# Kernel tuning notes

Measured on AMD Instinct MI355X. Metric: run time of the kernel, lower is better.

Reference implementation:

```python
import jax, jax.numpy as jnp
import numpy as np

B, N, C = 2, 2048, 1024
H = 16
D = C // H  # head_dim = 64
SCALE = D ** -0.5


def setup_inputs() -> dict:
    key = jax.random.key(0)
    k1, k2, k3, k4 = jax.random.split(key, 4)
    x = jax.random.normal(k1, (B, N, C), dtype=jnp.float32)
    # nn.Linear(in_dim, 3*out_dim, bias=False): store as [in, 3*out] for x @ W
    w_qkv = jax.random.normal(k2, (C, 3 * C), dtype=jnp.float32) * (C ** -0.5)
    w_proj = jax.random.normal(k3, (C, C), dtype=jnp.float32) * (C ** -0.5)
    b_proj = jax.random.normal(k4, (C,), dtype=jnp.float32) * 0.01
    return {"x": x, "w_qkv": w_qkv, "w_proj": w_proj, "b_proj": b_proj}


def reference(x, w_qkv, w_proj, b_proj):
    b, n, c = x.shape
    # QKV projection -> [3, B, H, N, D]
    qkv = (x @ w_qkv).reshape(b, n, 3, H, D).transpose(2, 0, 3, 1, 4)
    q, k, v = qkv[0], qkv[1], qkv[2]
    # scaled dot-product attention, full [B, H, N, N] scores as in original
    attn = jax.nn.softmax(jnp.einsum('bhqd,bhkd->bhqk', q * SCALE, k), axis=-1)
    out = jnp.einsum('bhqk,bhkd->bhqd', attn, v)  # [B, H, N, D]
    out = out.transpose(0, 2, 1, 3).reshape(b, n, c)
    return out @ w_proj + b_proj
```

## Files before the change

kernel.cpp:

```cpp
#include <hip/hip_runtime.h>

typedef unsigned short u16;
typedef float f32x4 __attribute__((ext_vector_type(4)));
typedef short bf16x8 __attribute__((ext_vector_type(8)));
typedef u16 u16x4 __attribute__((ext_vector_type(4)));
typedef u16 u16x8 __attribute__((ext_vector_type(8)));
typedef __bf16 bfr4 __attribute__((ext_vector_type(4)));

#define BB 2
#define NN 2048
#define CC 1024
#define HH 16
#define DD 64
#define MM (BB * NN)
#define NQKV (3 * CC)
#define QSCALE 0.18033688011112042f

#if __has_builtin(__builtin_amdgcn_exp2f)
#define EXP2(x) __builtin_amdgcn_exp2f(x)
#else
#define EXP2(x) exp2f(x)
#endif

__device__ __forceinline__ u16 f2bf(float f) {
    unsigned u = __float_as_uint(f);
    u += 0x7FFFu + ((u >> 16) & 1u);
    return (u16)(u >> 16);
}

__device__ __forceinline__ void ld_lds16(const u16* g, u16* l) {
    __builtin_amdgcn_global_load_lds(
        (const __attribute__((address_space(1))) unsigned int*)g,
        (__attribute__((address_space(3))) unsigned int*)l, 16, 0, 0);
}

__global__ __launch_bounds__(256) void k_tobf(const float* __restrict__ in,
                                              u16* __restrict__ out, int n) {
    int i = (blockIdx.x * 256 + threadIdx.x) * 8;
    if (i >= n) return;
    float4 a = *(const float4*)(in + i);
    float4 b = *(const float4*)(in + i + 4);
    u16x8 o;
    o[0] = f2bf(a.x); o[1] = f2bf(a.y); o[2] = f2bf(a.z); o[3] = f2bf(a.w);
    o[4] = f2bf(b.x); o[5] = f2bf(b.y); o[6] = f2bf(b.z); o[7] = f2bf(b.w);
    *(u16x8*)(out + i) = o;
}

__global__ __launch_bounds__(256) void k_tcast(const float* __restrict__ in,
                                               u16* __restrict__ out,
                                               int K, int Nn) {
    __shared__ float tile[32][33];
    int t = threadIdx.x, tx = t & 31, ty = t >> 5;
    int n0 = blockIdx.x * 32, k0 = blockIdx.y * 32;
#pragma unroll
    for (int r = 0; r < 32; r += 8)
        tile[ty + r][tx] = in[(size_t)(k0 + ty + r) * Nn + n0 + tx];
    __syncthreads();
#pragma unroll
    for (int r = 0; r < 32; r += 8)
        out[(size_t)(n0 + ty + r) * K + k0 + tx] = f2bf(tile[tx][ty + r]);
}

template <int MODE>
__global__ __launch_bounds__(256) void k_gemm(
    const u16* __restrict__ A, const u16* __restrict__ B,
    u16* __restrict__ Qb, u16* __restrict__ Kb, u16* __restrict__ Vb,
    const float* __restrict__ bias, float* __restrict__ Cout) {
    const int Kd = 1024;
    __shared__ __align__(16) u16 Ah[128][32];
    __shared__ __align__(16) u16 Bh[128][32];

    int t = threadIdx.x;
    int wave = t >> 6, lane = t & 63;
    int quad = lane >> 4, l16 = lane & 15;
    int wm = (wave >> 1) * 64, wn = (wave & 1) * 64;
    int m0 = blockIdx.y * 128, n0 = blockIdx.x * 128;

    int strow0 = wave * 16 + (lane >> 2);
    int stdst  = (lane & 3) * 8;
    int stsrc  = ((lane & 3) ^ ((lane >> 3) & 3)) * 8;
    int cfrag = (quad ^ ((l16 >> 1) & 3)) * 8;

    f32x4 acc[4][4];
#pragma unroll
    for (int i = 0; i < 4; i++)
#pragma unroll
        for (int j = 0; j < 4; j++) acc[i][j] = f32x4{0.f, 0.f, 0.f, 0.f};

    for (int k0 = 0; k0 < Kd; k0 += 32) {
        __syncthreads();
#pragma unroll
        for (int ii = 0; ii < 2; ii++) {
            int row = strow0 + ii * 64;
            ld_lds16(A + (size_t)(m0 + row) * Kd + k0 + stsrc, &Ah[row][stdst]);
            ld_lds16(B + (size_t)(n0 + row) * Kd + k0 + stsrc, &Bh[row][stdst]);
        }
        __syncthreads();

        bf16x8 af[4], bf[4];
#pragma unroll
        for (int i = 0; i < 4; i++) {
            af[i] = *(const bf16x8*)&Ah[wm + i * 16 + l16][cfrag];
            bf[i] = *(const bf16x8*)&Bh[wn + i * 16 + l16][cfrag];
        }
#pragma unroll
        for (int mi = 0; mi < 4; mi++)
#pragma unroll
            for (int ni = 0; ni < 4; ni++)
                acc[mi][ni] = __builtin_amdgcn_mfma_f32_16x16x32_bf16(
                    af[mi], bf[ni], acc[mi][ni], 0, 0, 0);
    }

#pragma unroll
    for (int mi = 0; mi < 4; mi++)
#pragma unroll
        for (int ni = 0; ni < 4; ni++)
#pragma unroll
            for (int r = 0; r < 4; r++) {
                int grow = m0 + wm + mi * 16 + quad * 4 + r;
                int gcol = n0 + wn + ni * 16 + l16;
                float v = acc[mi][ni][r];
                if (MODE == 0) {
                    int three = gcol >> 10, rem = gcol & 1023;
                    int h = rem >> 6, d = rem & 63;
                    int bb = grow >> 11, nn = grow & 2047;
                    if (three == 0) {
                        Qb[((size_t)(bb * HH + h) * NN + nn) * DD + d] = f2bf(v * QSCALE);
                    } else if (three == 1) {
                        Kb[((size_t)(bb * HH + h) * NN + nn) * DD + d] = f2bf(v);
                    } else {
                        Vb[((size_t)(bb * HH + h) * DD + d) * NN + nn] = f2bf(v);
                    }
                } else {
                    Cout[(size_t)grow * CC + gcol] = v + bias[gcol];
                }
            }
}

__global__ __launch_bounds__(512) void k_attn(const u16* __restrict__ Qb,
                                              const u16* __restrict__ Kb,
                                              const u16* __restrict__ VbT,
                                              u16* __restrict__ Ob) {
    __shared__ __align__(16) u16 Ks0[64][64], Ks1[64][64];
    __shared__ __align__(16) u16 Vs0[64][64], Vs1[64][64];
    __shared__ __align__(16) u16 Ps[8][16][72];

    int t = threadIdx.x, wave = t >> 6, lane = t & 63;
    int quad = lane >> 4, l16 = lane & 15;
    int bh = blockIdx.y, q0 = blockIdx.x * 128;
    const size_t kbase = (size_t)bh * NN * DD;
    const size_t vbase = (size_t)bh * DD * NN;

    int qrow = q0 + wave * 16 + l16;
    bf16x8 qf0 = *(const bf16x8*)&Qb[kbase + (size_t)qrow * DD + quad * 8];
    bf16x8 qf1 = *(const bf16x8*)&Qb[kbase + (size_t)qrow * DD + 32 + quad * 8];

    f32x4 o[4];
#pragma unroll
    for (int i = 0; i < 4; i++) o[i] = f32x4{0.f, 0.f, 0.f, 0.f};
    f32x4 lrow = f32x4{0.f, 0.f, 0.f, 0.f};

    int stgrp = lane & 7;
    int stsrc = (stgrp ^ (lane >> 3)) * 8;
    int strow = wave * 8 + (lane >> 3);
    int cf0 = (quad ^ (l16 & 7)) * 8;
    int cf1 = ((4 + quad) ^ (l16 & 7)) * 8;

    auto STAGE = [&](int cc, u16 (*Kd_)[64], u16 (*Vd_)[64]) {
        ld_lds16(&Kb[kbase + (size_t)(cc * 64 + strow) * DD + stsrc],
                 &Kd_[strow][stgrp * 8]);
        ld_lds16(&VbT[vbase + (size_t)strow * NN + cc * 64 + stsrc],
                 &Vd_[strow][stgrp * 8]);
    };

    auto COMPUTE = [&](u16 (*Ksrc)[64], u16 (*Vsrc)[64]) {
        bf16x8 kf[4][2];
#pragma unroll
        for (int kt = 0; kt < 4; kt++) {
            kf[kt][0] = *(const bf16x8*)&Ksrc[kt * 16 + l16][cf0];
            kf[kt][1] = *(const bf16x8*)&Ksrc[kt * 16 + l16][cf1];
        }
        f32x4 s[4];
        __builtin_amdgcn_s_setprio(1);
#pragma unroll
        for (int kt = 0; kt < 4; kt++) {
            f32x4 z = f32x4{0.f, 0.f, 0.f, 0.f};
            z = __builtin_amdgcn_mfma_f32_16x16x32_bf16(kf[kt][0], qf0, z, 0, 0, 0);
            z = __builtin_amdgcn_mfma_f32_16x16x32_bf16(kf[kt][1], qf1, z, 0, 0, 0);
            s[kt] = z;
        }
        __builtin_amdgcn_s_setprio(0);
#pragma unroll
        for (int kt = 0; kt < 4; kt++) {
            bfr4 pk;
#pragma unroll
            for (int r = 0; r < 4; r++) {
                float e = EXP2(s[kt][r]);
                lrow[r] += e;
                pk[r] = (__bf16)e;
            }
            *(bfr4*)&Ps[wave][l16][kt * 16 + quad * 4] = pk;
        }
        __asm__ volatile("s_waitcnt lgkmcnt(0)" ::: "memory");
        bf16x8 pb0 = *(const bf16x8*)&Ps[wave][l16][quad * 8];
        bf16x8 pb1 = *(const bf16x8*)&Ps[wave][l16][32 + quad * 8];
        __builtin_amdgcn_s_setprio(1);
#pragma unroll
        for (int dt = 0; dt < 4; dt++) {
            bf16x8 vf0 = *(const bf16x8*)&Vsrc[dt * 16 + l16][cf0];
            bf16x8 vf1 = *(const bf16x8*)&Vsrc[dt * 16 + l16][cf1];
            o[dt] = __builtin_amdgcn_mfma_f32_16x16x32_bf16(vf0, pb0, o[dt], 0, 0, 0);
            o[dt] = __builtin_amdgcn_mfma_f32_16x16x32_bf16(vf1, pb1, o[dt], 0, 0, 0);
        }
        __builtin_amdgcn_s_setprio(0);
    };

    STAGE(0, Ks0, Vs0);
    __syncthreads();

    for (int c = 0; c < NN / 64; c += 2) {
        STAGE(c + 1, Ks1, Vs1);
        COMPUTE(Ks0, Vs0);
        __syncthreads();
        if (c + 2 < NN / 64) STAGE(c + 2, Ks0, Vs0);
        COMPUTE(Ks1, Vs1);
        __syncthreads();
    }

    int b = bh >> 4, h = bh & 15;
    float l = (lrow[0] + lrow[1]) + (lrow[2] + lrow[3]);
    l += __shfl_xor(l, 16, 64);
    l += __shfl_xor(l, 32, 64);
    float inv = 1.f / l;
    int grow = b * NN + q0 + wave * 16 + l16;
#pragma unroll
    for (int dt = 0; dt < 4; dt++) {
        u16x4 hv;
#pragma unroll
        for (int r = 0; r < 4; r++) hv[r] = f2bf(o[dt][r] * inv);
        int gcol = h * DD + dt * 16 + quad * 4;
        *(u16x4*)&Ob[(size_t)grow * CC + gcol] = hv;
    }
}

extern "C" void kernel_launch(void* const* d_in, const int* in_sizes, int n_in,
                              void* d_out, int out_size, void* d_ws, size_t ws_size,
                              hipStream_t stream) {
    const float* x      = (const float*)d_in[0];
    const float* w_qkv  = (const float*)d_in[1];
    const float* w_proj = (const float*)d_in[2];
    const float* b_proj = (const float*)d_in[3];
    float* out = (float*)d_out;

    u16* p = (u16*)d_ws;
    u16* Xb = p; p += (size_t)MM * CC;
    u16* Wq = p; p += (size_t)NQKV * CC;
    u16* Wp = p; p += (size_t)CC * CC;
    u16* Qb = p; p += (size_t)MM * CC;
    u16* Kb = p; p += (size_t)MM * CC;
    u16* Vb = p; p += (size_t)MM * CC;
    u16* Ob = p; p += (size_t)MM * CC;

    k_tobf<<<(MM * CC) / (256 * 8), 256, 0, stream>>>(x, Xb, MM * CC);
    k_tcast<<<dim3(NQKV / 32, CC / 32), 256, 0, stream>>>(w_qkv, Wq, CC, NQKV);
    k_tcast<<<dim3(CC / 32, CC / 32), 256, 0, stream>>>(w_proj, Wp, CC, CC);
    k_gemm<0><<<dim3(NQKV / 128, MM / 128), 256, 0, stream>>>(
        Xb, Wq, Qb, Kb, Vb, nullptr, nullptr);
    k_attn<<<dim3(NN / 128, BB * HH), 512, 0, stream>>>(Qb, Kb, Vb, Ob);
    k_gemm<1><<<dim3(CC / 128, MM / 128), 256, 0, stream>>>(
        Ob, Wp, nullptr, nullptr, nullptr, b_proj, out);
}
```

Measured before the change: 191.4 us.

## Fuse prep casts into one kernel and double-buffer GEMM with 512 threads

Merges the x cast and the two weight transpose-casts into a single launch, removing two kernel launches. The GEMM now uses 8 waves per block with a 64x32 per-wave tile and double-buffered LDS, so the next K slice is loaded while the current one is computed and one barrier per slice is dropped. This raises occupancy and overlap. In exchange, each wave reads more LDS per MFMA and the block uses twice the shared memory.

```diff
diff --git a/kernel.cpp b/kernel.cpp
--- a/kernel.cpp
+++ b/kernel.cpp
@@ -34,87 +34,107 @@
         (__attribute__((address_space(3))) unsigned int*)l, 16, 0, 0);
 }
 
-__global__ __launch_bounds__(256) void k_tobf(const float* __restrict__ in,
-                                              u16* __restrict__ out, int n) {
-    int i = (blockIdx.x * 256 + threadIdx.x) * 8;
-    if (i >= n) return;
-    float4 a = *(const float4*)(in + i);
-    float4 b = *(const float4*)(in + i + 4);
-    u16x8 o;
-    o[0] = f2bf(a.x); o[1] = f2bf(a.y); o[2] = f2bf(a.z); o[3] = f2bf(a.w);
-    o[4] = f2bf(b.x); o[5] = f2bf(b.y); o[6] = f2bf(b.z); o[7] = f2bf(b.w);
-    *(u16x8*)(out + i) = o;
-}
-
-__global__ __launch_bounds__(256) void k_tcast(const float* __restrict__ in,
-                                               u16* __restrict__ out,
-                                               int K, int Nn) {
+__global__ __launch_bounds__(256) void k_prep(const float* __restrict__ x,
+                                              const float* __restrict__ wqkv,
+                                              const float* __restrict__ wproj,
+                                              u16* __restrict__ Xb,
+                                              u16* __restrict__ Wq,
+                                              u16* __restrict__ Wp) {
     __shared__ float tile[32][33];
-    int t = threadIdx.x, tx = t & 31, ty = t >> 5;
-    int n0 = blockIdx.x * 32, k0 = blockIdx.y * 32;
+    int bid = blockIdx.x, t = threadIdx.x;
+    if (bid < 2048) {
+        int i = (bid * 256 + t) * 8;
+        float4 a = *(const float4*)(x + i);
+        float4 b = *(const float4*)(x + i + 4);
+        u16x8 o;
+        o[0] = f2bf(a.x); o[1] = f2bf(a.y); o[2] = f2bf(a.z); o[3] = f2bf(a.w);
+        o[4] = f2bf(b.x); o[5] = f2bf(b.y); o[6] = f2bf(b.z); o[7] = f2bf(b.w);
+        *(u16x8*)(Xb + i) = o;
+        return;
+    }
+    const float* in;
+    u16* out;
+    int Nn, n0, k0;
+    if (bid < 2048 + 3072) {
+        int b2 = bid - 2048;
+        in = wqkv; out = Wq; Nn = NQKV;
+        n0 = (b2 % 96) * 32; k0 = (b2 / 96) * 32;
+    } else {
+        int b3 = bid - 5120;
+        in = wproj; out = Wp; Nn = CC;
+        n0 = (b3 & 31) * 32; k0 = (b3 >> 5) * 32;
+    }
+    int tx = t & 31, ty = t >> 5;
 #pragma unroll
     for (int r = 0; r < 32; r += 8)
         tile[ty + r][tx] = in[(size_t)(k0 + ty + r) * Nn + n0 + tx];
     __syncthreads();
 #pragma unroll
     for (int r = 0; r < 32; r += 8)
-        out[(size_t)(n0 + ty + r) * K + k0 + tx] = f2bf(tile[tx][ty + r]);
+        out[(size_t)(n0 + ty + r) * CC + k0 + tx] = f2bf(tile[tx][ty + r]);
 }
 
 template <int MODE>
-__global__ __launch_bounds__(256) void k_gemm(
+__global__ __launch_bounds__(512) void k_gemm(
     const u16* __restrict__ A, const u16* __restrict__ B,
     u16* __restrict__ Qb, u16* __restrict__ Kb, u16* __restrict__ Vb,
     const float* __restrict__ bias, float* __restrict__ Cout) {
     const int Kd = 1024;
-    __shared__ __align__(16) u16 Ah[128][32];
-    __shared__ __align__(16) u16 Bh[128][32];
+    __shared__ __align__(16) u16 Ah0[128][32], Ah1[128][32];
+    __shared__ __align__(16) u16 Bh0[128][32], Bh1[128][32];
 
     int t = threadIdx.x;
     int wave = t >> 6, lane = t & 63;
     int quad = lane >> 4, l16 = lane & 15;
-    int wm = (wave >> 1) * 64, wn = (wave & 1) * 64;
+    int wm = (wave >> 2) * 64, wn = (wave & 3) * 32;
     int m0 = blockIdx.y * 128, n0 = blockIdx.x * 128;
 
-    int strow0 = wave * 16 + (lane >> 2);
-    int stdst  = (lane & 3) * 8;
-    int stsrc  = ((lane & 3) ^ ((lane >> 3) & 3)) * 8;
+    int strow = wave * 16 + (lane >> 2);
+    int stdst = (lane & 3) * 8;
+    int stsrc = ((lane & 3) ^ ((lane >> 3) & 3)) * 8;
     int cfrag = (quad ^ ((l16 >> 1) & 3)) * 8;
 
-    f32x4 acc[4][4];
+    f32x4 acc[4][2];
 #pragma unroll
     for (int i = 0; i < 4; i++)
 #pragma unroll
-        for (int j = 0; j < 4; j++) acc[i][j] = f32x4{0.f, 0.f, 0.f, 0.f};
-
-    for (int k0 = 0; k0 < Kd; k0 += 32) {
-        __syncthreads();
-#pragma unroll
-        for (int ii = 0; ii < 2; ii++) {
-            int row = strow0 + ii * 64;
-            ld_lds16(A + (size_t)(m0 + row) * Kd + k0 + stsrc, &Ah[row][stdst]);
-            ld_lds16(B + (size_t)(n0 + row) * Kd + k0 + stsrc, &Bh[row][stdst]);
-        }
-        __syncthreads();
-
-        bf16x8 af[4], bf[4];
-#pragma unroll
-        for (int i = 0; i < 4; i++) {
-            af[i] = *(const bf16x8*)&Ah[wm + i * 16 + l16][cfrag];
-            bf[i] = *(const bf16x8*)&Bh[wn + i * 16 + l16][cfrag];
-        }
+        for (int j = 0; j < 2; j++) acc[i][j] = f32x4{0.f, 0.f, 0.f, 0.f};
+
+    auto STAGE = [&](int k0, u16 (*Ad)[32], u16 (*Bd)[32]) {
+        ld_lds16(A + (size_t)(m0 + strow) * Kd + k0 + stsrc, &Ad[strow][stdst]);
+        ld_lds16(B + (size_t)(n0 + strow) * Kd + k0 + stsrc, &Bd[strow][stdst]);
+    };
+    auto COMPUTE = [&](u16 (*As)[32], u16 (*Bs)[32]) {
+        bf16x8 af[4], bf[2];
+#pragma unroll
+        for (int i = 0; i < 4; i++)
+            af[i] = *(const bf16x8*)&As[wm + i * 16 + l16][cfrag];
+#pragma unroll
+        for (int j = 0; j < 2; j++)
+            bf[j] = *(const bf16x8*)&Bs[wn + j * 16 + l16][cfrag];
 #pragma unroll
         for (int mi = 0; mi < 4; mi++)
 #pragma unroll
-            for (int ni = 0; ni < 4; ni++)
+            for (int ni = 0; ni < 2; ni++)
                 acc[mi][ni] = __builtin_amdgcn_mfma_f32_16x16x32_bf16(
                     af[mi], bf[ni], acc[mi][ni], 0, 0, 0);
+    };
+
+    STAGE(0, Ah0, Bh0);
+    __syncthreads();
+    for (int k0 = 0; k0 < Kd; k0 += 64) {
+        STAGE(k0 + 32, Ah1, Bh1);
+        COMPUTE(Ah0, Bh0);
+        __syncthreads();
+        if (k0 + 64 < Kd) STAGE(k0 + 64, Ah0, Bh0);
+        COMPUTE(Ah1, Bh1);
+        __syncthreads();
     }
 
 #pragma unroll
     for (int mi = 0; mi < 4; mi++)
 #pragma unroll
-        for (int ni = 0; ni < 4; ni++)
+        for (int ni = 0; ni < 2; ni++)
 #pragma unroll
             for (int r = 0; r < 4; r++) {
                 int grow = m0 + wm + mi * 16 + quad * 4 + r;
@@ -261,12 +281,10 @@
     u16* Vb = p; p += (size_t)MM * CC;
     u16* Ob = p; p += (size_t)MM * CC;
 
-    k_tobf<<<(MM * CC) / (256 * 8), 256, 0, stream>>>(x, Xb, MM * CC);
-    k_tcast<<<dim3(NQKV / 32, CC / 32), 256, 0, stream>>>(w_qkv, Wq, CC, NQKV);
-    k_tcast<<<dim3(CC / 32, CC / 32), 256, 0, stream>>>(w_proj, Wp, CC, CC);
-    k_gemm<0><<<dim3(NQKV / 128, MM / 128), 256, 0, stream>>>(
+    k_prep<<<2048 + 3072 + 1024, 256, 0, stream>>>(x, w_qkv, w_proj, Xb, Wq, Wp);
+    k_gemm<0><<<dim3(NQKV / 128, MM / 128), 512, 0, stream>>>(
         Xb, Wq, Qb, Kb, Vb, nullptr, nullptr);
     k_attn<<<dim3(NN / 128, BB * HH), 512, 0, stream>>>(Qb, Kb, Vb, Ob);
-    k_gemm<1><<<dim3(CC / 128, MM / 128), 256, 0, stream>>>(
+    k_gemm<1><<<dim3(CC / 128, MM / 128), 512, 0, stream>>>(
         Ob, Wp, nullptr, nullptr, nullptr, b_proj, out);
 }
```

New measurement: 197.3 us. 3.1% more time.
